# Optimization experiments

Hardware: AMD Instinct MI355X
Metric: run time of the kernel (lower is better)

Reference implementation:

```python
import jax, jax.numpy as jnp
import numpy as np

B = 16384
C = 2048  # in_channel
OUT = 2   # out_channel


def setup_inputs() -> dict:
    key = jax.random.key(0)
    k1, k2, k3, k4, k5, k6, k7 = jax.random.split(key, 7)
    scale = 1.0 / np.sqrt(3 * C)  # torch Linear default init range
    return {
        "s_f": jax.random.normal(k1, (B, C), dtype=jnp.float32),
        "g_f": jax.random.normal(k2, (B, C), dtype=jnp.float32),
        "v_f": jax.random.normal(k3, (B, C), dtype=jnp.float32),
        "W_aff": jax.random.uniform(k4, (3 * C, 3), dtype=jnp.float32, minval=-scale, maxval=scale),
        "b_aff": jax.random.uniform(k5, (3,), dtype=jnp.float32, minval=-scale, maxval=scale),
        "W_cls": jax.random.uniform(k6, (3 * C, OUT), dtype=jnp.float32, minval=-scale, maxval=scale),
        "b_cls": jax.random.uniform(k7, (OUT,), dtype=jnp.float32, minval=-scale, maxval=scale),
    }


def reference(s_f, g_f, v_f, W_aff, b_aff, W_cls, b_cls):
    # Attention gating over the three modalities.
    x_att = jnp.concatenate([s_f, g_f, v_f], axis=1)          # [B, 3C]
    att = jax.nn.softmax(x_att @ W_aff + b_aff, axis=1)       # [B, 3]
    # diag(att[:, i]) @ f  ==  per-row scalar scaling (broadcast multiply).
    s = att[:, 0:1] * s_f
    g = att[:, 1:2] * g_f
    v = att[:, 2:3] * v_f
    x = jnp.concatenate([s, g, v], axis=1)                    # [B, 3C]
    return jax.nn.softmax(x @ W_cls + b_cls, axis=1)          # [B, OUT]
```

## Files before the change

kernel.cpp:

```cpp
#include <hip/hip_runtime.h>

#define B_ROWS 16384
#define C_DIM  2048
#define BLK    256
#define CPT    8
#define RPB    32
#define GROUP  8
#define NACC   5

#define DPP_ADD(v, ctrl, rmask) \
  v += __int_as_float(__builtin_amdgcn_update_dpp(0, __float_as_int(v), (ctrl), (rmask), 0xf, false))

__device__ __forceinline__ float wave_sum64(float v) {
  DPP_ADD(v, 0x111, 0xf);
  DPP_ADD(v, 0x112, 0xf);
  DPP_ADD(v, 0x114, 0xf);
  DPP_ADD(v, 0x118, 0xf);
  DPP_ADD(v, 0x142, 0xa);
  DPP_ADD(v, 0x143, 0xc);
  return v;
}

__global__ __launch_bounds__(BLK, 6)
void maff_partial(const float* __restrict__ s_f,
                  const float* __restrict__ g_f,
                  const float* __restrict__ v_f,
                  const float* __restrict__ W_aff,
                  const float* __restrict__ W_cls,
                  float* __restrict__ ws)
{
  const int t    = threadIdx.x;
  const int lane = t & 63;
  const int wave = t >> 6;
  const int m    = blockIdx.y;
  const int row0 = blockIdx.x * RPB;
  const int c0   = t * CPT;

  const float* f = (m == 0) ? s_f : (m == 1) ? g_f : v_f;

  float wa[CPT][3];
  float wc[CPT][2];
  {
    const float4* pa = (const float4*)(W_aff + ((size_t)m * C_DIM + c0) * 3);
    float4 a0 = pa[0], a1 = pa[1], a2 = pa[2], a3 = pa[3], a4 = pa[4], a5 = pa[5];
    wa[0][0]=a0.x; wa[0][1]=a0.y; wa[0][2]=a0.z;
    wa[1][0]=a0.w; wa[1][1]=a1.x; wa[1][2]=a1.y;
    wa[2][0]=a1.z; wa[2][1]=a1.w; wa[2][2]=a2.x;
    wa[3][0]=a2.y; wa[3][1]=a2.z; wa[3][2]=a2.w;
    wa[4][0]=a3.x; wa[4][1]=a3.y; wa[4][2]=a3.z;
    wa[5][0]=a3.w; wa[5][1]=a4.x; wa[5][2]=a4.y;
    wa[6][0]=a4.z; wa[6][1]=a4.w; wa[6][2]=a5.x;
    wa[7][0]=a5.y; wa[7][1]=a5.z; wa[7][2]=a5.w;
    const float4* pc = (const float4*)(W_cls + ((size_t)m * C_DIM + c0) * 2);
    float4 q0 = pc[0], q1 = pc[1], q2 = pc[2], q3 = pc[3];
    wc[0][0]=q0.x; wc[0][1]=q0.y; wc[1][0]=q0.z; wc[1][1]=q0.w;
    wc[2][0]=q1.x; wc[2][1]=q1.y; wc[3][0]=q1.z; wc[3][1]=q1.w;
    wc[4][0]=q2.x; wc[4][1]=q2.y; wc[5][0]=q2.z; wc[5][1]=q2.w;
    wc[6][0]=q3.x; wc[6][1]=q3.y; wc[7][0]=q3.z; wc[7][1]=q3.w;
  }

  __shared__ float red[2][GROUP][4][NACC];

  const float* b0 = f + (size_t)row0 * C_DIM + c0;
  float4 cx0 = ((const float4*)b0)[0];
  float4 cx1 = ((const float4*)b0)[1];

  for (int r = 0; r < RPB; ++r) {
    const int    nr = (r + 1 < RPB) ? (r + 1) : r;
    const float* nb = f + (size_t)(row0 + nr) * C_DIM + c0;
    float4 nx0 = ((const float4*)nb)[0];
    float4 nx1 = ((const float4*)nb)[1];

    float x[CPT] = {cx0.x, cx0.y, cx0.z, cx0.w, cx1.x, cx1.y, cx1.z, cx1.w};

    float p0 = 0.f, p1 = 0.f, p2 = 0.f, q0 = 0.f, q1 = 0.f;
#pragma unroll
    for (int i = 0; i < CPT; ++i) {
      p0 = fmaf(x[i], wa[i][0], p0);
      p1 = fmaf(x[i], wa[i][1], p1);
      p2 = fmaf(x[i], wa[i][2], p2);
      q0 = fmaf(x[i], wc[i][0], q0);
      q1 = fmaf(x[i], wc[i][1], q1);
    }

    p0 = wave_sum64(p0); p1 = wave_sum64(p1); p2 = wave_sum64(p2);
    q0 = wave_sum64(q0); q1 = wave_sum64(q1);

    const int gs = r & (GROUP - 1);
    const int gb = (r >> 3) & 1;
    if (lane == 63) {
      float* d = &red[gb][gs][wave][0];
      d[0] = p0; d[1] = p1; d[2] = p2; d[3] = q0; d[4] = q1;
    }

    if (gs == GROUP - 1) {
      __syncthreads();
      if (t < GROUP) {
        const float* z = &red[gb][t][0][0];
        float s0 = z[0] + z[5] + z[10] + z[15];
        float s1 = z[1] + z[6] + z[11] + z[16];
        float s2 = z[2] + z[7] + z[12] + z[17];
        float s3 = z[3] + z[8] + z[13] + z[18];
        float s4 = z[4] + z[9] + z[14] + z[19];
        const int row = row0 + (r - (GROUP - 1)) + t;
        ws[(m * 5 + 0) * B_ROWS + row] = s0;
        ws[(m * 5 + 1) * B_ROWS + row] = s1;
        ws[(m * 5 + 2) * B_ROWS + row] = s2;
        ws[(m * 5 + 3) * B_ROWS + row] = s3;
        ws[(m * 5 + 4) * B_ROWS + row] = s4;
      }
    }

    cx0 = nx0; cx1 = nx1;
  }
}

__global__ __launch_bounds__(BLK)
void maff_epilogue(const float* __restrict__ ws,
                   const float* __restrict__ b_aff,
                   const float* __restrict__ b_cls,
                   float* __restrict__ out)
{
  const int row = blockIdx.x * BLK + threadIdx.x;

  float P[3][NACC];
#pragma unroll
  for (int m = 0; m < 3; ++m)
#pragma unroll
    for (int j = 0; j < NACC; ++j)
      P[m][j] = ws[(m * NACC + j) * B_ROWS + row];

  float A0 = P[0][0] + P[1][0] + P[2][0] + b_aff[0];
  float A1 = P[0][1] + P[1][1] + P[2][1] + b_aff[1];
  float A2 = P[0][2] + P[1][2] + P[2][2] + b_aff[2];

  float mx = fmaxf(A0, fmaxf(A1, A2));
  float e0 = __expf(A0 - mx), e1 = __expf(A1 - mx), e2 = __expf(A2 - mx);
  float inv = 1.0f / (e0 + e1 + e2);
  float t0 = e0 * inv, t1 = e1 * inv, t2 = e2 * inv;

  float L0 = t0 * P[0][3] + t1 * P[1][3] + t2 * P[2][3] + b_cls[0];
  float L1 = t0 * P[0][4] + t1 * P[1][4] + t2 * P[2][4] + b_cls[1];
  float mm = fmaxf(L0, L1);
  float x0 = __expf(L0 - mm), x1 = __expf(L1 - mm);
  float is = 1.0f / (x0 + x1);

  *(float2*)(out + (size_t)row * 2) = make_float2(x0 * is, x1 * is);
}

extern "C" void kernel_launch(void* const* d_in, const int* in_sizes, int n_in,
                              void* d_out, int out_size, void* d_ws, size_t ws_size,
                              hipStream_t stream) {
  const float* s_f   = (const float*)d_in[0];
  const float* g_f   = (const float*)d_in[1];
  const float* v_f   = (const float*)d_in[2];
  const float* W_aff = (const float*)d_in[3];
  const float* b_aff = (const float*)d_in[4];
  const float* W_cls = (const float*)d_in[5];
  const float* b_cls = (const float*)d_in[6];
  float* out = (float*)d_out;
  float* ws  = (float*)d_ws;

  dim3 grid1(B_ROWS / RPB, 3);
  maff_partial<<<grid1, dim3(BLK), 0, stream>>>(s_f, g_f, v_f, W_aff, W_cls, ws);

  dim3 grid2(B_ROWS / BLK);
  maff_epilogue<<<grid2, dim3(BLK), 0, stream>>>(ws, b_aff, b_cls, out);
}
```

Measured before the change: 366.3 us.

## Widen blocks, batch four rows per iteration, reduce within 16-lane groups

Each thread now covers 4 columns with 512 threads per block. Four rows are loaded and double-buffered per iteration, so more loads are in flight at once. The cross-row DPP reduction is cut to 16-lane sums, and partials from 32 slots per row are summed through shared memory. This aims to raise memory-level parallelism and cut shuffle work, at the cost of more shared-memory traffic and more serial summation in a few threads, plus an occupancy change from dropping the min-blocks hint.

```diff
diff --git a/kernel.cpp b/kernel.cpp
--- a/kernel.cpp
+++ b/kernel.cpp
@@ -2,26 +2,27 @@
 
 #define B_ROWS 16384
 #define C_DIM  2048
-#define BLK    256
-#define CPT    8
+#define BLK    512
+#define CPT    4
 #define RPB    32
+#define RB     4
+#define NITER  (RPB / RB)
 #define GROUP  8
+#define NWAVE  (BLK / 64)
 #define NACC   5
 
 #define DPP_ADD(v, ctrl, rmask) \
   v += __int_as_float(__builtin_amdgcn_update_dpp(0, __float_as_int(v), (ctrl), (rmask), 0xf, false))
 
-__device__ __forceinline__ float wave_sum64(float v) {
+__device__ __forceinline__ float wave_sum16(float v) {
   DPP_ADD(v, 0x111, 0xf);
   DPP_ADD(v, 0x112, 0xf);
   DPP_ADD(v, 0x114, 0xf);
   DPP_ADD(v, 0x118, 0xf);
-  DPP_ADD(v, 0x142, 0xa);
-  DPP_ADD(v, 0x143, 0xc);
   return v;
 }
 
-__global__ __launch_bounds__(BLK, 6)
+__global__ __launch_bounds__(BLK)
 void maff_partial(const float* __restrict__ s_f,
                   const float* __restrict__ g_f,
                   const float* __restrict__ v_f,
@@ -32,6 +33,7 @@
   const int t    = threadIdx.x;
   const int lane = t & 63;
   const int wave = t >> 6;
+  const int grp  = lane >> 4;
   const int m    = blockIdx.y;
   const int row0 = blockIdx.x * RPB;
   const int c0   = t * CPT;
@@ -42,86 +44,98 @@
   float wc[CPT][2];
   {
     const float4* pa = (const float4*)(W_aff + ((size_t)m * C_DIM + c0) * 3);
-    float4 a0 = pa[0], a1 = pa[1], a2 = pa[2], a3 = pa[3], a4 = pa[4], a5 = pa[5];
+    float4 a0 = pa[0], a1 = pa[1], a2 = pa[2];
     wa[0][0]=a0.x; wa[0][1]=a0.y; wa[0][2]=a0.z;
     wa[1][0]=a0.w; wa[1][1]=a1.x; wa[1][2]=a1.y;
     wa[2][0]=a1.z; wa[2][1]=a1.w; wa[2][2]=a2.x;
     wa[3][0]=a2.y; wa[3][1]=a2.z; wa[3][2]=a2.w;
-    wa[4][0]=a3.x; wa[4][1]=a3.y; wa[4][2]=a3.z;
-    wa[5][0]=a3.w; wa[5][1]=a4.x; wa[5][2]=a4.y;
-    wa[6][0]=a4.z; wa[6][1]=a4.w; wa[6][2]=a5.x;
-    wa[7][0]=a5.y; wa[7][1]=a5.z; wa[7][2]=a5.w;
     const float4* pc = (const float4*)(W_cls + ((size_t)m * C_DIM + c0) * 2);
-    float4 q0 = pc[0], q1 = pc[1], q2 = pc[2], q3 = pc[3];
+    float4 q0 = pc[0], q1 = pc[1];
     wc[0][0]=q0.x; wc[0][1]=q0.y; wc[1][0]=q0.z; wc[1][1]=q0.w;
     wc[2][0]=q1.x; wc[2][1]=q1.y; wc[3][0]=q1.z; wc[3][1]=q1.w;
-    wc[4][0]=q2.x; wc[4][1]=q2.y; wc[5][0]=q2.z; wc[5][1]=q2.w;
-    wc[6][0]=q3.x; wc[6][1]=q3.y; wc[7][0]=q3.z; wc[7][1]=q3.w;
   }
 
-  __shared__ float red[2][GROUP][4][NACC];
+  __shared__ float red[2][GROUP][NWAVE][4][NACC];
 
-  const float* b0 = f + (size_t)row0 * C_DIM + c0;
-  float4 cx0 = ((const float4*)b0)[0];
-  float4 cx1 = ((const float4*)b0)[1];
+  const float* base = f + (size_t)row0 * C_DIM + c0;
 
-  for (int r = 0; r < RPB; ++r) {
-    const int    nr = (r + 1 < RPB) ? (r + 1) : r;
-    const float* nb = f + (size_t)(row0 + nr) * C_DIM + c0;
-    float4 nx0 = ((const float4*)nb)[0];
-    float4 nx1 = ((const float4*)nb)[1];
+  float4 cur[RB];
+#pragma unroll
+  for (int k = 0; k < RB; ++k)
+    cur[k] = *(const float4*)(base + (size_t)k * C_DIM);
 
-    float x[CPT] = {cx0.x, cx0.y, cx0.z, cx0.w, cx1.x, cx1.y, cx1.z, cx1.w};
+  for (int it = 0; it < NITER; ++it) {
+    const int nit = (it + 1 < NITER) ? (it + 1) : it;
+    float4 nxt[RB];
+#pragma unroll
+    for (int k = 0; k < RB; ++k)
+      nxt[k] = *(const float4*)(base + (size_t)(nit * RB + k) * C_DIM);
 
-    float p0 = 0.f, p1 = 0.f, p2 = 0.f, q0 = 0.f, q1 = 0.f;
+    float acc[RB][NACC];
 #pragma unroll
-    for (int i = 0; i < CPT; ++i) {
-      p0 = fmaf(x[i], wa[i][0], p0);
-      p1 = fmaf(x[i], wa[i][1], p1);
-      p2 = fmaf(x[i], wa[i][2], p2);
-      q0 = fmaf(x[i], wc[i][0], q0);
-      q1 = fmaf(x[i], wc[i][1], q1);
+    for (int k = 0; k < RB; ++k) {
+      float x[CPT] = {cur[k].x, cur[k].y, cur[k].z, cur[k].w};
+      float p0 = 0.f, p1 = 0.f, p2 = 0.f, q0 = 0.f, q1 = 0.f;
+#pragma unroll
+      for (int i = 0; i < CPT; ++i) {
+        p0 = fmaf(x[i], wa[i][0], p0);
+        p1 = fmaf(x[i], wa[i][1], p1);
+        p2 = fmaf(x[i], wa[i][2], p2);
+        q0 = fmaf(x[i], wc[i][0], q0);
+        q1 = fmaf(x[i], wc[i][1], q1);
+      }
+      acc[k][0] = p0; acc[k][1] = p1; acc[k][2] = p2;
+      acc[k][3] = q0; acc[k][4] = q1;
     }
 
-    p0 = wave_sum64(p0); p1 = wave_sum64(p1); p2 = wave_sum64(p2);
-    q0 = wave_sum64(q0); q1 = wave_sum64(q1);
+#pragma unroll
+    for (int k = 0; k < RB; ++k)
+#pragma unroll
+      for (int j = 0; j < NACC; ++j)
+        acc[k][j] = wave_sum16(acc[k][j]);
 
-    const int gs = r & (GROUP - 1);
-    const int gb = (r >> 3) & 1;
-    if (lane == 63) {
-      float* d = &red[gb][gs][wave][0];
-      d[0] = p0; d[1] = p1; d[2] = p2; d[3] = q0; d[4] = q1;
-    }
-
-    if (gs == GROUP - 1) {
-      __syncthreads();
-      if (t < GROUP) {
-        const float* z = &red[gb][t][0][0];
-        float s0 = z[0] + z[5] + z[10] + z[15];
-        float s1 = z[1] + z[6] + z[11] + z[16];
-        float s2 = z[2] + z[7] + z[12] + z[17];
-        float s3 = z[3] + z[8] + z[13] + z[18];
-        float s4 = z[4] + z[9] + z[14] + z[19];
-        const int row = row0 + (r - (GROUP - 1)) + t;
-        ws[(m * 5 + 0) * B_ROWS + row] = s0;
-        ws[(m * 5 + 1) * B_ROWS + row] = s1;
-        ws[(m * 5 + 2) * B_ROWS + row] = s2;
-        ws[(m * 5 + 3) * B_ROWS + row] = s3;
-        ws[(m * 5 + 4) * B_ROWS + row] = s4;
+    const int g  = it >> 1;
+    const int gb = g & 1;
+#pragma unroll
+    for (int k = 0; k < RB; ++k) {
+      const int r  = it * RB + k;
+      const int gs = r & (GROUP - 1);
+      if ((lane & 15) == 15) {
+        float* d = &red[gb][gs][wave][grp][0];
+        d[0] = acc[k][0]; d[1] = acc[k][1]; d[2] = acc[k][2];
+        d[3] = acc[k][3]; d[4] = acc[k][4];
       }
     }
 
-    cx0 = nx0; cx1 = nx1;
+    if (it & 1) {
+      __syncthreads();
+      if (t < GROUP) {
+        float s[NACC] = {0.f, 0.f, 0.f, 0.f, 0.f};
+        const float* z = &red[gb][t][0][0][0];
+#pragma unroll
+        for (int w = 0; w < NWAVE * 4; ++w)
+#pragma unroll
+          for (int j = 0; j < NACC; ++j)
+            s[j] += z[w * NACC + j];
+        const int row = row0 + g * GROUP + t;
+#pragma unroll
+        for (int j = 0; j < NACC; ++j)
+          ws[(m * NACC + j) * B_ROWS + row] = s[j];
+      }
+    }
+
+#pragma unroll
+    for (int k = 0; k < RB; ++k) cur[k] = nxt[k];
   }
 }
 
-__global__ __launch_bounds__(BLK)
+__global__ __launch_bounds__(256)
 void maff_epilogue(const float* __restrict__ ws,
                    const float* __restrict__ b_aff,
                    const float* __restrict__ b_cls,
                    float* __restrict__ out)
 {
-  const int row = blockIdx.x * BLK + threadIdx.x;
+  const int row = blockIdx.x * 256 + threadIdx.x;
 
   float P[3][NACC];
 #pragma unroll
@@ -164,6 +178,6 @@
   dim3 grid1(B_ROWS / RPB, 3);
   maff_partial<<<grid1, dim3(BLK), 0, stream>>>(s_f, g_f, v_f, W_aff, W_cls, ws);
 
-  dim3 grid2(B_ROWS / BLK);
-  maff_epilogue<<<grid2, dim3(BLK), 0, stream>>>(ws, b_aff, b_cls, out);
+  dim3 grid2(B_ROWS / 256);
+  maff_epilogue<<<grid2, dim3(256), 0, stream>>>(ws, b_aff, b_cls, out);
 }
```

Measured after the change: 363.2 us. About the same (-0.9%).
